# Optimization experiments

Hardware: AMD Instinct MI355X
Metric: run time of the kernel (lower is better)

Reference implementation:

```python
import jax, jax.numpy as jnp
import numpy as np

EPS = 1e-12

def _l2norm(x):
    # F.normalize(p=2, dim=-1) semantics: x / max(||x||, eps)
    n = jnp.sqrt(jnp.sum(x * x, axis=-1, keepdims=True))
    return x / jnp.maximum(n, EPS)

def _split_heads(x, h):
    b, l, d = x.shape
    return x.reshape(b, l, h, d // h).transpose(0, 2, 1, 3)  # (B,H,L,dh)

def _join_heads(x):
    b, h, l, dh = x.shape
    return x.transpose(0, 2, 1, 3).reshape(b, l, h * dh)

def setup_inputs() -> dict:
    key = jax.random.key(0)
    B, L, D = 4, 4096, 1024
    ks = jax.random.split(key, 12)
    s = 1.0 / np.sqrt(D)
    inp = {
        "queries": jax.random.normal(ks[0], (B, L, D), jnp.float32),
        "values": jax.random.normal(ks[1], (B, L, D), jnp.float32),
        "keys": jax.random.normal(ks[2], (B, L, D), jnp.float32),
        "key_attention_mask": jnp.ones((B, L), jnp.float32),
        "Wq": jax.random.uniform(ks[3], (D, D), jnp.float32, -s, s),
        "bq": jax.random.uniform(ks[4], (D,), jnp.float32, -s, s),
        "Wk": jax.random.uniform(ks[5], (D, D), jnp.float32, -s, s),
        "bk": jax.random.uniform(ks[6], (D,), jnp.float32, -s, s),
        "Wv": jax.random.uniform(ks[7], (D, D), jnp.float32, -s, s),
        "bv": jax.random.uniform(ks[8], (D,), jnp.float32, -s, s),
        "Wo": jax.random.uniform(ks[9], (D, D), jnp.float32, -s, s),
        "bo": jax.random.uniform(ks[10], (D,), jnp.float32, -s, s),
    }
    return inp

def reference(queries, values, keys, key_attention_mask, Wq, bq, Wk, bk, Wv, bv, Wo, bo):
    nhead = 16
    L2 = keys.shape[1]
    qp = jnp.einsum('bld,ed->ble', queries, Wq) + bq
    kp = jnp.einsum('bld,ed->ble', keys, Wk) + bk
    vp = jnp.einsum('bld,ed->ble', values, Wv) + bv
    Q = _split_heads(qp, nhead)   # (B,H,L1,dh)
    K = _split_heads(kp, nhead)   # (B,H,L2,dh)
    V = _split_heads(vp, nhead)   # (B,H,L2,dh)
    V_minus = jnp.minimum(V, 0.0)
    V_plus = jnp.maximum(V, 0.0)
    Q = jax.nn.sigmoid(Q)
    scaled_K = jax.nn.sigmoid(K) / L2
    # AmplitudeEmbedding: L2-normalize feature maps along feature dim
    Q = _l2norm(Q)
    scaled_K = _l2norm(scaled_K)
    kv_plus = jnp.einsum('bhld,bhlc,bl->bhdc', scaled_K, V_plus, key_attention_mask)
    heads_plus = _l2norm(jnp.einsum('bhld,bhdc->bhlc', Q, kv_plus))
    kv_minus = jnp.einsum('bhld,bhlc,bl->bhdc', scaled_K, V_minus, key_attention_mask)
    heads_minus = _l2norm(jnp.einsum('bhld,bhdc->bhlc', Q, kv_minus))
    out = _join_heads(heads_plus + heads_minus)  # (B,L1,D)
    return jnp.einsum('blc,dc->bld', out, Wo) + bo
```

## Files before the change

### kernel.cpp

```cpp
#include <hip/hip_runtime.h>
#include <stdint.h>

#define B_  4
#define L_  4096
#define D_  1024
#define H_  16
#define DH  64
#define M_  (B_*L_)

typedef _Float16 f16;
typedef __attribute__((ext_vector_type(8))) _Float16 f16x8;
typedef __attribute__((ext_vector_type(4))) _Float16 f16x4;
typedef __attribute__((ext_vector_type(4))) float    f32x4;

__device__ __forceinline__ void cp16(const void* g, void* l) {
  __builtin_amdgcn_global_load_lds(
      (const __attribute__((address_space(1))) void*)g,
      (__attribute__((address_space(3))) void*)l,
      16, 0, 0);
}

#define MFMA(a,b,c) __builtin_amdgcn_mfma_f32_16x16x32_f16(a,b,c,0,0,0)

#define PH_IN do { __builtin_amdgcn_s_barrier(); \
  asm volatile("s_waitcnt lgkmcnt(0)" ::: "memory"); \
  __builtin_amdgcn_sched_barrier(0); \
  __builtin_amdgcn_s_setprio(1); } while (0)
#define PH_OUT do { __builtin_amdgcn_s_setprio(0); \
  __builtin_amdgcn_sched_barrier(0); \
  asm volatile("" ::: "memory"); \
  __builtin_amdgcn_s_barrier(); } while (0)
#define PH_OUT_VM(nimm) do { __builtin_amdgcn_s_setprio(0); \
  __builtin_amdgcn_sched_barrier(0); \
  asm volatile("s_waitcnt vmcnt(" #nimm ")" ::: "memory"); \
  __builtin_amdgcn_s_barrier(); } while (0)

__global__ __launch_bounds__(256) void k_cvt_f16(const float* __restrict__ x,
                                                 f16* __restrict__ y, int n8) {
  int i = blockIdx.x * 256 + threadIdx.x;
  if (i >= n8) return;
  const float4* xv = (const float4*)x;
  float4 a = xv[2*i], b = xv[2*i+1];
  f16x8 o;
  o[0]=(f16)a.x; o[1]=(f16)a.y; o[2]=(f16)a.z; o[3]=(f16)a.w;
  o[4]=(f16)b.x; o[5]=(f16)b.y; o[6]=(f16)b.z; o[7]=(f16)b.w;
  ((f16x8*)y)[i] = o;
}

__global__ __launch_bounds__(256) void k_split_w(const float* __restrict__ x,
                                                 f16* __restrict__ cat, int n4) {
  int i = blockIdx.x * 256 + threadIdx.x;
  if (i >= n4) return;
  float4 a = ((const float4*)x)[i];
  int n  = i >> 8;
  int k4 = i & 255;
  f16 h0=(f16)a.x, h1=(f16)a.y, h2=(f16)a.z, h3=(f16)a.w;
  f16x4 hv = {h0, h1, h2, h3};
  f16x4 lv = {(f16)(a.x-(float)h0), (f16)(a.y-(float)h1),
              (f16)(a.z-(float)h2), (f16)(a.w-(float)h3)};
  size_t rh = (size_t)((n >> 4) * 32 + (n & 15));
  ((f16x4*)cat)[rh * 256 + k4]        = hv;
  ((f16x4*)cat)[(rh + 16) * 256 + k4] = lv;
}

__global__ __launch_bounds__(512, 2) void k_gemm8(
    const f16* __restrict__ A, const f16* __restrict__ Bw,
    const float* __restrict__ bias, const float* __restrict__ mask,
    float* __restrict__ Cf, f16* __restrict__ Ch, int mode,
    int M, int N, int K) {
  __shared__ __align__(16) char sA[65536];
  __shared__ __align__(16) char sB[65536];
  const int t = threadIdx.x;
  const int nbn = N >> 8;
  int bid = blockIdx.x;
  {
    int cpx = (int)gridDim.x >> 3;
    bid = (bid & 7) * cpx + (bid >> 3);
  }
  const int bm = (bid / nbn) << 8;
  const int bn = (bid % nbn) << 8;
  const int lane = t & 63, wave = t >> 6;
  const int wm = wave >> 2;
  const int wn = wave & 3;
  const int fm = lane & 15, fkb = lane >> 4;

  auto SA_ = [&](int T, int buf, int half) {
#pragma unroll
    for (int q = 0; q < 2; ++q) {
      int li = (q << 9) + t;
      int row = li >> 3, cb = li & 7;
      const f16* g = A + (size_t)(bm + (half << 7) + row) * K
                       + (T << 6) + ((cb ^ (row & 7)) << 3);
      cp16(g, sA + buf * 32768 + half * 16384 + li * 16);
    }
  };
  auto SB_ = [&](int T, int buf, int half) {
#pragma unroll
    for (int q = 0; q < 2; ++q) {
      int li = (q << 9) + t;
      int row = li >> 3, cb = li & 7;
      const f16* g = Bw + (size_t)(bn + (half << 7) + row) * K
                        + (T << 6) + ((cb ^ (row & 7)) << 3);
      cp16(g, sB + buf * 32768 + half * 16384 + li * 16);
    }
  };
  auto LDA = [&](int buf, int i, int ks) -> f16x8 {
    int row = (i << 4) + fm;
    int blk = ((ks << 2) + fkb) ^ (row & 7);
    return *(const f16x8*)(sA + buf * 32768 + (wm << 14) + (row << 7) + (blk << 4));
  };
  auto LDB = [&](int buf, int j, int ks) -> f16x8 {
    int row = ((wn & 1) << 6) + (j << 4) + fm;
    int blk = ((ks << 2) + fkb) ^ (row & 7);
    return *(const f16x8*)(sB + buf * 32768 + ((wn >> 1) << 14) + (row << 7) + (blk << 4));
  };

  f32x4 acc[8][4] = {};

  SA_(0, 0, 0); SA_(0, 0, 1);
  SB_(0, 0, 0); SB_(0, 0, 1);
  SB_(1, 1, 0); SB_(1, 1, 1);
  asm volatile("s_waitcnt vmcnt(4)" ::: "memory");
  __builtin_amdgcn_s_barrier();

  const int NI = K >> 7;
  for (int it = 0; it < NI; ++it) {
    const bool nl = (it != NI - 1);
    const int t2 = 2 * it + 2, t3 = 2 * it + 3;
    f16x8 aL[4][2], aH[4][2], bA[2][2], bB[2][2];

#pragma unroll
    for (int i = 0; i < 4; ++i) { aL[i][0] = LDA(0,i,0); aL[i][1] = LDA(0,i,1); }
#pragma unroll
    for (int j = 0; j < 2; ++j) { bA[j][0] = LDB(0,j,0); bA[j][1] = LDB(0,j,1); }
    SA_(2*it+1, 1, 0);
    PH_IN;
#pragma unroll
    for (int i = 0; i < 4; ++i)
#pragma unroll
      for (int j = 0; j < 2; ++j) {
        acc[i][j] = MFMA(aL[i][0], bA[j][0], acc[i][j]);
        acc[i][j] = MFMA(aL[i][1], bA[j][1], acc[i][j]);
      }
    PH_OUT;
#pragma unroll
    for (int j = 0; j < 2; ++j) { bB[j][0] = LDB(0,j+2,0); bB[j][1] = LDB(0,j+2,1); }
    SA_(2*it+1, 1, 1);
    PH_IN;
#pragma unroll
    for (int i = 0; i < 4; ++i)
#pragma unroll
      for (int j = 0; j < 2; ++j) {
        acc[i][j+2] = MFMA(aL[i][0], bB[j][0], acc[i][j+2]);
        acc[i][j+2] = MFMA(aL[i][1], bB[j][1], acc[i][j+2]);
      }
    PH_OUT;
#pragma unroll
    for (int i = 0; i < 4; ++i) { aH[i][0] = LDA(0,i+4,0); aH[i][1] = LDA(0,i+4,1); }
    if (nl) SB_(t2, 0, 0);
    PH_IN;
#pragma unroll
    for (int i = 0; i < 4; ++i)
#pragma unroll
      for (int j = 0; j < 2; ++j) {
        acc[i+4][j] = MFMA(aH[i][0], bA[j][0], acc[i+4][j]);
        acc[i+4][j] = MFMA(aH[i][1], bA[j][1], acc[i+4][j]);
      }
    PH_OUT;
    if (nl) SB_(t2, 0, 1);
    PH_IN;
#pragma unroll
    for (int i = 0; i < 4; ++i)
#pragma unroll
      for (int j = 0; j < 2; ++j) {
        acc[i+4][j+2] = MFMA(aH[i][0], bB[j][0], acc[i+4][j+2]);
        acc[i+4][j+2] = MFMA(aH[i][1], bB[j][1], acc[i+4][j+2]);
      }
    if (nl) PH_OUT_VM(4); else PH_OUT_VM(0);
#pragma unroll
    for (int i = 0; i < 4; ++i) { aL[i][0] = LDA(1,i,0); aL[i][1] = LDA(1,i,1); }
#pragma unroll
    for (int j = 0; j < 2; ++j) { bA[j][0] = LDB(1,j,0); bA[j][1] = LDB(1,j,1); }
    if (nl) SA_(t2, 0, 0);
    PH_IN;
#pragma unroll
    for (int i = 0; i < 4; ++i)
#pragma unroll
      for (int j = 0; j < 2; ++j) {
        acc[i][j] = MFMA(aL[i][0], bA[j][0], acc[i][j]);
        acc[i][j] = MFMA(aL[i][1], bA[j][1], acc[i][j]);
      }
    PH_OUT;
#pragma unroll
    for (int j = 0; j < 2; ++j) { bB[j][0] = LDB(1,j+2,0); bB[j][1] = LDB(1,j+2,1); }
    if (nl) SA_(t2, 0, 1);
    PH_IN;
#pragma unroll
    for (int i = 0; i < 4; ++i)
#pragma unroll
      for (int j = 0; j < 2; ++j) {
        acc[i][j+2] = MFMA(aL[i][0], bB[j][0], acc[i][j+2]);
        acc[i][j+2] = MFMA(aL[i][1], bB[j][1], acc[i][j+2]);
      }
    PH_OUT;
#pragma unroll
    for (int i = 0; i < 4; ++i) { aH[i][0] = LDA(1,i+4,0); aH[i][1] = LDA(1,i+4,1); }
    if (nl) SB_(t3, 1, 0);
    PH_IN;
#pragma unroll
    for (int i = 0; i < 4; ++i)
#pragma unroll
      for (int j = 0; j < 2; ++j) {
        acc[i+4][j] = MFMA(aH[i][0], bA[j][0], acc[i+4][j]);
        acc[i+4][j] = MFMA(aH[i][1], bA[j][1], acc[i+4][j]);
      }
    PH_OUT;
    if (nl) SB_(t3, 1, 1);
    PH_IN;
#pragma unroll
    for (int i = 0; i < 4; ++i)
#pragma unroll
      for (int j = 0; j < 2; ++j) {
        acc[i+4][j+2] = MFMA(aH[i][0], bB[j][0], acc[i+4][j+2]);
        acc[i+4][j+2] = MFMA(aH[i][1], bB[j][1], acc[i+4][j+2]);
      }
    PH_OUT_VM(4);
  }

  const int cr = (lane >> 4) << 2, ccol = lane & 15;
  const int rowbase = bm + wm * 128;
  if (mode == 1) {
    const int No = N;
    float bvj[4];
#pragma unroll
    for (int j = 0; j < 4; ++j) bvj[j] = bias[bn + wn*64 + j*16 + ccol];
#pragma unroll
    for (int i = 0; i < 8; ++i)
#pragma unroll
      for (int r = 0; r < 4; ++r) {
        int gm = rowbase + i*16 + cr + r;
        float s[4], ss = 0.f;
#pragma unroll
        for (int j = 0; j < 4; ++j) {
          float v = acc[i][j][r] + bvj[j];
          s[j] = 1.0f / (1.0f + __expf(-v));
          ss += s[j] * s[j];
        }
        ss += __shfl_xor(ss, 1, 64);
        ss += __shfl_xor(ss, 2, 64);
        ss += __shfl_xor(ss, 4, 64);
        ss += __shfl_xor(ss, 8, 64);
        float sc = 1.0f / fmaxf(sqrtf(ss), 1e-12f);
        if (mask) sc *= mask[gm];
#pragma unroll
        for (int j = 0; j < 4; ++j)
          Ch[(size_t)gm * No + bn + wn*64 + j*16 + ccol] = (f16)(s[j] * sc);
      }
  } else {
    const int No = N >> 1;
#pragma unroll
    for (int j2 = 0; j2 < 2; ++j2) {
      int colp = bn + wn*64 + (2*j2)*16;
      int oc = ((colp >> 5) << 4) + ccol;
      float bv = bias[oc];
#pragma unroll
      for (int i = 0; i < 8; ++i)
#pragma unroll
        for (int r = 0; r < 4; ++r) {
          int gm = rowbase + i*16 + cr + r;
          float v = acc[i][2*j2][r] + acc[i][2*j2+1][r] + bv;
          if (mode == 2) Ch[(size_t)gm * No + oc] = (f16)v;
          else           Cf[(size_t)gm * No + oc] = v;
        }
    }
  }
}

#define SKT 72
__global__ __launch_bounds__(256) void k_kv_mfma(const f16* __restrict__ Kh,
                                                 const f16* __restrict__ Vh,
                                                 float* __restrict__ part) {
  __shared__ __align__(16) f16 sKt[64 * SKT];
  __shared__ __align__(16) f16 sVt[128 * SKT];
  int head = blockIdx.x >> 3, chunk = blockIdx.x & 7;
  int b = head >> 4, h = head & 15;
  int t = threadIdx.x, lane = t & 63, wave = t >> 6;
  int lp = t & 31, g8 = (t >> 5) << 3;
  size_t rowbase = (size_t)b * L_ + (size_t)chunk * 512;
  const f16* Kb = Kh + rowbase * D_ + h * DH;
  const f16* Vb = Vh + rowbase * D_ + h * DH;

  const int fm = lane & 15, fk = (lane >> 4) << 3;
  const int wm2 = (wave & 1) * 2;
  const int wn4 = (wave >> 1) * 4;
  f32x4 acc[2][4] = {};

  for (int l0 = 0; l0 < 512; l0 += 64) {
    __syncthreads();
    {
      const f16* r0 = Kb + (size_t)(l0 + 2*lp) * D_ + g8;
      f16x8 a0 = *(const f16x8*)r0;
      f16x8 a1 = *(const f16x8*)(r0 + D_);
#pragma unroll
      for (int j = 0; j < 8; ++j) {
        union { f16 h2[2]; uint32_t u; } pk;
        pk.h2[0] = a0[j]; pk.h2[1] = a1[j];
        *(uint32_t*)&sKt[(g8 + j) * SKT + 2*lp] = pk.u;
      }
      const f16* v0p = Vb + (size_t)(l0 + 2*lp) * D_ + g8;
      f16x8 b0 = *(const f16x8*)v0p;
      f16x8 b1 = *(const f16x8*)(v0p + D_);
#pragma unroll
      for (int j = 0; j < 8; ++j) {
        float x0 = (float)b0[j], x1 = (float)b1[j];
        union { f16 h2[2]; uint32_t u; } pp, pm;
        pp.h2[0] = (f16)fmaxf(x0, 0.f); pp.h2[1] = (f16)fmaxf(x1, 0.f);
        pm.h2[0] = (f16)fminf(x0, 0.f); pm.h2[1] = (f16)fminf(x1, 0.f);
        *(uint32_t*)&sVt[(g8 + j) * SKT + 2*lp]        = pp.u;
        *(uint32_t*)&sVt[(64 + g8 + j) * SKT + 2*lp]   = pm.u;
      }
    }
    __syncthreads();
#pragma unroll
    for (int ks = 0; ks < 2; ++ks) {
      f16x8 af[2], bf[4];
#pragma unroll
      for (int i = 0; i < 2; ++i)
        af[i] = *(const f16x8*)&sKt[((wm2+i)*16 + fm) * SKT + ks*32 + fk];
#pragma unroll
      for (int j = 0; j < 4; ++j)
        bf[j] = *(const f16x8*)&sVt[((wn4+j)*16 + fm) * SKT + ks*32 + fk];
#pragma unroll
      for (int i = 0; i < 2; ++i)
#pragma unroll
        for (int j = 0; j < 4; ++j)
          acc[i][j] = MFMA(af[i], bf[j], acc[i][j]);
    }
  }
  const int cr = (lane >> 4) << 2, ccol = lane & 15;
  float* pb = part + (size_t)(head * 8 + chunk) * 8192;
#pragma unroll
  for (int i = 0; i < 2; ++i)
#pragma unroll
    for (int j = 0; j < 4; ++j) {
      int d = (wm2 + i) * 16 + cr;
      int c2 = (wn4 + j) * 16 + ccol;
#pragma unroll
      for (int r = 0; r < 4; ++r)
        pb[(d + r) * 128 + c2] = acc[i][j][r];
    }
}

__global__ __launch_bounds__(256) void k_kv_reduce(const float* __restrict__ part,
                                                   float* __restrict__ kv) {
  int i = blockIdx.x * 256 + threadIdx.x;
  int head = i >> 13, dc = i & 8191;
  float s = 0.f;
#pragma unroll
  for (int c = 0; c < 8; ++c) s += part[(size_t)(head * 8 + c) * 8192 + dc];
  kv[i] = s;
}

__global__ __launch_bounds__(256) void k_kv_cvt(const float* __restrict__ kvb,
                                                f16* __restrict__ kvh) {
  int head = blockIdx.x, t = threadIdx.x;
  int c = t >> 1, half = t & 1;
  const float* src = kvb + (size_t)head * 8192 + half * 32 * 128 + c;
  f16* dst = kvh + (size_t)head * 8192 + c * 64 + half * 32;
  f16 buf[32];
#pragma unroll
  for (int kk = 0; kk < 32; ++kk) buf[kk] = (f16)src[kk * 128];
#pragma unroll
  for (int q = 0; q < 4; ++q) ((f16x8*)dst)[q] = *(const f16x8*)&buf[q * 8];
}

#define SH 72
__global__ __launch_bounds__(256) void k_heads_mfma(const f16* __restrict__ Qh,
                                                    const f16* __restrict__ kvh,
                                                    f16* __restrict__ O) {
  __shared__ __align__(16) f16 sQ [128 * SH];
  __shared__ __align__(16) f16 sKV[128 * SH];
  int bi = blockIdx.x;
  int head = bi >> 5, mt = bi & 31;
  int b = head >> 4, h = head & 15;
  int t = threadIdx.x, lane = t & 63, wave = t >> 6;
  size_t qbase = ((size_t)(b * L_ + mt * 128)) * D_ + h * DH;
  const f16* kvp = kvh + (size_t)head * 8192;
#pragma unroll
  for (int p = 0; p < 4; ++p) {
    int c = p * 256 + t;
    int row = c >> 3, off = (c & 7) * 8;
    f16x8 q = *(const f16x8*)(Qh + qbase + (size_t)row * D_ + off);
    *(f16x8*)&sQ[row * SH + off] = q;
    f16x8 kv8 = *(const f16x8*)(kvp + row * 64 + off);
    *(f16x8*)&sKV[row * SH + off] = kv8;
  }
  __syncthreads();

  const int fm = lane & 15, fk = (lane >> 4) << 3;
  const int wm = wave * 32;
  f32x4 acc[2][8] = {};
#pragma unroll
  for (int ks = 0; ks < 2; ++ks) {
    f16x8 a0 = *(const f16x8*)&sQ[(wm + fm) * SH + ks * 32 + fk];
    f16x8 a1 = *(const f16x8*)&sQ[(wm + 16 + fm) * SH + ks * 32 + fk];
#pragma unroll
    for (int j = 0; j < 8; ++j) {
      f16x8 bj = *(const f16x8*)&sKV[(j * 16 + fm) * SH + ks * 32 + fk];
      acc[0][j] = MFMA(a0, bj, acc[0][j]);
      acc[1][j] = MFMA(a1, bj, acc[1][j]);
    }
  }
  const int cr = (lane >> 4) << 2, ccol = lane & 15;
#pragma unroll
  for (int i = 0; i < 2; ++i)
#pragma unroll
    for (int r = 0; r < 4; ++r) {
      int row = wm + i * 16 + cr + r;
      float sp = 0.f, sm = 0.f;
#pragma unroll
      for (int j = 0; j < 4; ++j) {
        sp += acc[i][j][r] * acc[i][j][r];
        sm += acc[i][j + 4][r] * acc[i][j + 4][r];
      }
      sp += __shfl_xor(sp, 1, 64); sm += __shfl_xor(sm, 1, 64);
      sp += __shfl_xor(sp, 2, 64); sm += __shfl_xor(sm, 2, 64);
      sp += __shfl_xor(sp, 4, 64); sm += __shfl_xor(sm, 4, 64);
      sp += __shfl_xor(sp, 8, 64); sm += __shfl_xor(sm, 8, 64);
      float rp = 1.0f / fmaxf(sqrtf(sp), 1e-12f);
      float rm = 1.0f / fmaxf(sqrtf(sm), 1e-12f);
#pragma unroll
      for (int j = 0; j < 4; ++j) {
        float o = acc[i][j][r] * rp + acc[i][j + 4][r] * rm;
        O[qbase + (size_t)row * D_ + j * 16 + ccol] = (f16)o;
      }
    }
}

extern "C" void kernel_launch(void* const* d_in, const int* in_sizes, int n_in,
                              void* d_out, int out_size, void* d_ws, size_t ws_size,
                              hipStream_t stream) {
  const float* queries = (const float*)d_in[0];
  const float* values  = (const float*)d_in[1];
  const float* keys    = (const float*)d_in[2];
  const float* mask    = (const float*)d_in[3];
  const float* Wq = (const float*)d_in[4];  const float* bq = (const float*)d_in[5];
  const float* Wk = (const float*)d_in[6];  const float* bk = (const float*)d_in[7];
  const float* Wv = (const float*)d_in[8];  const float* bv = (const float*)d_in[9];
  const float* Wo = (const float*)d_in[10]; const float* bo = (const float*)d_in[11];
  float* out = (float*)d_out;

  const size_t MB = 1024ull * 1024ull;
  const size_t NEED = 160 * MB;
  if (ws_size < NEED) return;

  char* ws = (char*)d_ws;
  const size_t DD = (size_t)D_ * D_;
  f16*   Wqh  = (f16*)(ws);
  f16*   Wkh  = (f16*)(ws + 2 * MB);
  f16*   Wcv  = (f16*)(ws + 4 * MB);
  f16*   Wco  = (f16*)(ws + 8 * MB);
  f16*   Ah   = (f16*)(ws + 12 * MB);
  f16*   Qh   = (f16*)(ws + 44 * MB);
  float* kvb  = (float*)(ws + 76 * MB);
  f16*   kvh  = (f16*)(ws + 78 * MB);
  float* part = (float*)(ws + 80 * MB);
  f16*   kp   = (f16*)(ws + 96 * MB);
  f16*   vp   = (f16*)(ws + 128 * MB);

  const int DD8 = (int)(DD / 8);
  const int DD4 = (int)(DD / 4);
  k_cvt_f16<<<DD8 / 256, 256, 0, stream>>>(Wq, Wqh, DD8);
  k_cvt_f16<<<DD8 / 256, 256, 0, stream>>>(Wk, Wkh, DD8);
  k_split_w<<<DD4 / 256, 256, 0, stream>>>(Wv, Wcv, DD4);
  k_split_w<<<DD4 / 256, 256, 0, stream>>>(Wo, Wco, DD4);

  const int n8 = M_ * D_ / 8;
  const int g1 = (M_ / 256) * (1024 / 256);
  const int g2 = (M_ / 256) * (2048 / 256);

  k_cvt_f16<<<n8 / 256, 256, 0, stream>>>(queries, Ah, n8);
  k_gemm8<<<g1, 512, 0, stream>>>(Ah, Wqh, bq, nullptr, nullptr, Qh, 1, M_, 1024, 1024);
  k_cvt_f16<<<n8 / 256, 256, 0, stream>>>(keys, Ah, n8);
  k_gemm8<<<g1, 512, 0, stream>>>(Ah, Wkh, bk, mask, nullptr, kp, 1, M_, 1024, 1024);
  k_cvt_f16<<<n8 / 256, 256, 0, stream>>>(values, Ah, n8);
  k_gemm8<<<g2, 512, 0, stream>>>(Ah, Wcv, bv, nullptr, nullptr, vp, 2, M_, 2048, 1024);

  k_kv_mfma<<<64 * 8, 256, 0, stream>>>(kp, vp, part);
  k_kv_reduce<<<64 * 8192 / 256, 256, 0, stream>>>(part, kvb);
  k_kv_cvt<<<64, 256, 0, stream>>>(kvb, kvh);
  k_heads_mfma<<<64 * 32, 256, 0, stream>>>(Qh, kvh, Ah);

  k_gemm8<<<g2, 512, 0, stream>>>(Ah, Wco, bo, nullptr, out, nullptr, 3, M_, 2048, 1024);
}
```

Measured before the change: 554.6 us.

## Stage GEMM epilogues through LDS, batch Q/K GEMMs, and merge small kernels

```diff
diff --git a/kernel.cpp b/kernel.cpp
--- a/kernel.cpp
+++ b/kernel.cpp
@@ -47,10 +47,23 @@
   ((f16x8*)y)[i] = o;
 }
 
-__global__ __launch_bounds__(256) void k_split_w(const float* __restrict__ x,
-                                                 f16* __restrict__ cat, int n4) {
+__global__ __launch_bounds__(256) void k_cvt2(const float* __restrict__ x0,
+                                              f16* __restrict__ y0,
+                                              const float* __restrict__ x1,
+                                              f16* __restrict__ y1, int n8each) {
   int i = blockIdx.x * 256 + threadIdx.x;
-  if (i >= n4) return;
+  const float* x = x0; f16* y = y0;
+  if (i >= n8each) { x = x1; y = y1; i -= n8each; }
+  const float4* xv = (const float4*)x;
+  float4 a = xv[2*i], b = xv[2*i+1];
+  f16x8 o;
+  o[0]=(f16)a.x; o[1]=(f16)a.y; o[2]=(f16)a.z; o[3]=(f16)a.w;
+  o[4]=(f16)b.x; o[5]=(f16)b.y; o[6]=(f16)b.z; o[7]=(f16)b.w;
+  ((f16x8*)y)[i] = o;
+}
+
+__device__ __forceinline__ void split_one(const float* __restrict__ x,
+                                          f16* __restrict__ cat, int i) {
   float4 a = ((const float4*)x)[i];
   int n  = i >> 8;
   int k4 = i & 255;
@@ -63,18 +76,35 @@
   ((f16x4*)cat)[(rh + 16) * 256 + k4] = lv;
 }
 
-__global__ __launch_bounds__(512, 2) void k_gemm8(
-    const f16* __restrict__ A, const f16* __restrict__ Bw,
-    const float* __restrict__ bias, const float* __restrict__ mask,
-    float* __restrict__ Cf, f16* __restrict__ Ch, int mode,
-    int M, int N, int K) {
-  __shared__ __align__(16) char sA[65536];
-  __shared__ __align__(16) char sB[65536];
+__global__ __launch_bounds__(256) void k_split2(const float* __restrict__ x0,
+                                                f16* __restrict__ c0,
+                                                const float* __restrict__ x1,
+                                                f16* __restrict__ c1, int n4each) {
+  int i = blockIdx.x * 256 + threadIdx.x;
+  if (i < n4each) split_one(x0, c0, i);
+  else            split_one(x1, c1, i - n4each);
+}
+
+struct GemmJob {
+  const f16* A; const f16* Bw; const float* bias; const float* mask;
+  float* Cf; f16* Ch; int mode; int N;
+};
+
+__global__ __launch_bounds__(512, 2) void k_gemm8(GemmJob j0, GemmJob j1,
+                                                  int nblk0, int M, int K) {
+  __shared__ __align__(16) char smem[137216];
+  char* sA = smem;
+  char* sB = smem + 65536;
   const int t = threadIdx.x;
+
+  int raw = (int)blockIdx.x;
+  GemmJob J; int bid, nblk;
+  if (raw < nblk0) { J = j0; bid = raw;         nblk = nblk0; }
+  else             { J = j1; bid = raw - nblk0; nblk = (int)gridDim.x - nblk0; }
+  const int N = J.N;
   const int nbn = N >> 8;
-  int bid = blockIdx.x;
   {
-    int cpx = (int)gridDim.x >> 3;
+    int cpx = nblk >> 3;
     bid = (bid & 7) * cpx + (bid >> 3);
   }
   const int bm = (bid / nbn) << 8;
@@ -84,13 +114,15 @@
   const int wn = wave & 3;
   const int fm = lane & 15, fkb = lane >> 4;
 
+  const f16* Ab = J.A;
+  const f16* Bb = J.Bw;
   auto SA_ = [&](int T, int buf, int half) {
 #pragma unroll
     for (int q = 0; q < 2; ++q) {
       int li = (q << 9) + t;
       int row = li >> 3, cb = li & 7;
-      const f16* g = A + (size_t)(bm + (half << 7) + row) * K
-                       + (T << 6) + ((cb ^ (row & 7)) << 3);
+      const f16* g = Ab + (size_t)(bm + (half << 7) + row) * K
+                        + (T << 6) + ((cb ^ (row & 7)) << 3);
       cp16(g, sA + buf * 32768 + half * 16384 + li * 16);
     }
   };
@@ -99,7 +131,7 @@
     for (int q = 0; q < 2; ++q) {
       int li = (q << 9) + t;
       int row = li >> 3, cb = li & 7;
-      const f16* g = Bw + (size_t)(bn + (half << 7) + row) * K
+      const f16* g = Bb + (size_t)(bn + (half << 7) + row) * K
                         + (T << 6) + ((cb ^ (row & 7)) << 3);
       cp16(g, sB + buf * 32768 + half * 16384 + li * 16);
     }
@@ -229,49 +261,75 @@
 
   const int cr = (lane >> 4) << 2, ccol = lane & 15;
   const int rowbase = bm + wm * 128;
-  if (mode == 1) {
-    const int No = N;
+  float* sOut = (float*)smem;
+  if (J.mode == 1) {
     float bvj[4];
 #pragma unroll
-    for (int j = 0; j < 4; ++j) bvj[j] = bias[bn + wn*64 + j*16 + ccol];
-#pragma unroll
-    for (int i = 0; i < 8; ++i)
-#pragma unroll
-      for (int r = 0; r < 4; ++r) {
-        int gm = rowbase + i*16 + cr + r;
-        float s[4], ss = 0.f;
-#pragma unroll
-        for (int j = 0; j < 4; ++j) {
-          float v = acc[i][j][r] + bvj[j];
-          s[j] = 1.0f / (1.0f + __expf(-v));
-          ss += s[j] * s[j];
+    for (int j = 0; j < 4; ++j) bvj[j] = J.bias[bn + wn*64 + j*16 + ccol];
+    for (int h = 0; h < 2; ++h) {
+      if (wm == h) {
+#pragma unroll
+        for (int i = 0; i < 8; ++i)
+#pragma unroll
+          for (int r = 0; r < 4; ++r) {
+            int rl = i*16 + cr + r;
+            int gm = rowbase + rl;
+            float s[4], ss = 0.f;
+#pragma unroll
+            for (int j = 0; j < 4; ++j) {
+              float v = acc[i][j][r] + bvj[j];
+              s[j] = 1.0f / (1.0f + __expf(-v));
+              ss += s[j] * s[j];
+            }
+            ss += __shfl_xor(ss, 1, 64);
+            ss += __shfl_xor(ss, 2, 64);
+            ss += __shfl_xor(ss, 4, 64);
+            ss += __shfl_xor(ss, 8, 64);
+            float sc = 1.0f / fmaxf(sqrtf(ss), 1e-12f);
+            if (J.mask) sc *= J.mask[gm];
+#pragma unroll
+            for (int j = 0; j < 4; ++j)
+              sOut[rl*268 + wn*64 + j*16 + ccol] = s[j] * sc;
+          }
+      }
+      __syncthreads();
+#pragma unroll
+      for (int sp = 0; sp < 16; ++sp) {
+        int rl = sp*8 + (t >> 6);
+        int c4 = (t & 63) * 4;
+        f32x4 v = *(const f32x4*)&sOut[rl*268 + c4];
+        f16x4 o = {(f16)v[0], (f16)v[1], (f16)v[2], (f16)v[3]};
+        *(f16x4*)&J.Ch[(size_t)(bm + h*128 + rl) * N + bn + c4] = o;
+      }
+      __syncthreads();
+    }
+  } else {
+#pragma unroll
+    for (int j2 = 0; j2 < 2; ++j2) {
+      int ocl = wn*32 + j2*16 + ccol;
+      float bv = J.bias[(bn >> 1) + ocl];
+#pragma unroll
+      for (int i = 0; i < 8; ++i)
+#pragma unroll
+        for (int r = 0; r < 4; ++r) {
+          int rl = wm*128 + i*16 + cr + r;
+          sOut[rl*132 + ocl] = acc[i][2*j2][r] + acc[i][2*j2+1][r] + bv;
         }
-        ss += __shfl_xor(ss, 1, 64);
-        ss += __shfl_xor(ss, 2, 64);
-        ss += __shfl_xor(ss, 4, 64);
-        ss += __shfl_xor(ss, 8, 64);
-        float sc = 1.0f / fmaxf(sqrtf(ss), 1e-12f);
-        if (mask) sc *= mask[gm];
-#pragma unroll
-        for (int j = 0; j < 4; ++j)
-          Ch[(size_t)gm * No + bn + wn*64 + j*16 + ccol] = (f16)(s[j] * sc);
-      }
-  } else {
+    }
+    __syncthreads();
     const int No = N >> 1;
 #pragma unroll
-    for (int j2 = 0; j2 < 2; ++j2) {
-      int colp = bn + wn*64 + (2*j2)*16;
-      int oc = ((colp >> 5) << 4) + ccol;
-      float bv = bias[oc];
-#pragma unroll
-      for (int i = 0; i < 8; ++i)
-#pragma unroll
-        for (int r = 0; r < 4; ++r) {
-          int gm = rowbase + i*16 + cr + r;
-          float v = acc[i][2*j2][r] + acc[i][2*j2+1][r] + bv;
-          if (mode == 2) Ch[(size_t)gm * No + oc] = (f16)v;
-          else           Cf[(size_t)gm * No + oc] = v;
-        }
+    for (int sp = 0; sp < 16; ++sp) {
+      int rl = sp*16 + (t >> 5);
+      int c4 = (t & 31) * 4;
+      f32x4 v = *(const f32x4*)&sOut[rl*132 + c4];
+      size_t g = (size_t)(bm + rl) * No + (bn >> 1) + c4;
+      if (J.mode == 2) {
+        f16x4 o = {(f16)v[0], (f16)v[1], (f16)v[2], (f16)v[3]};
+        *(f16x4*)&J.Ch[g] = o;
+      } else {
+        *(f32x4*)&J.Cf[g] = v;
+      }
     }
   }
 }
@@ -351,25 +409,20 @@
     }
 }
 
-__global__ __launch_bounds__(256) void k_kv_reduce(const float* __restrict__ part,
-                                                   float* __restrict__ kv) {
-  int i = blockIdx.x * 256 + threadIdx.x;
-  int head = i >> 13, dc = i & 8191;
-  float s = 0.f;
-#pragma unroll
-  for (int c = 0; c < 8; ++c) s += part[(size_t)(head * 8 + c) * 8192 + dc];
-  kv[i] = s;
-}
-
-__global__ __launch_bounds__(256) void k_kv_cvt(const float* __restrict__ kvb,
-                                                f16* __restrict__ kvh) {
+__global__ __launch_bounds__(256) void k_kv_redcvt(const float* __restrict__ part,
+                                                   f16* __restrict__ kvh) {
   int head = blockIdx.x, t = threadIdx.x;
   int c = t >> 1, half = t & 1;
-  const float* src = kvb + (size_t)head * 8192 + half * 32 * 128 + c;
+  const float* src = part + (size_t)head * 8 * 8192 + half * 32 * 128 + c;
   f16* dst = kvh + (size_t)head * 8192 + c * 64 + half * 32;
   f16 buf[32];
 #pragma unroll
-  for (int kk = 0; kk < 32; ++kk) buf[kk] = (f16)src[kk * 128];
+  for (int kk = 0; kk < 32; ++kk) {
+    float s = 0.f;
+#pragma unroll
+    for (int ch = 0; ch < 8; ++ch) s += src[(size_t)ch * 8192 + kk * 128];
+    buf[kk] = (f16)s;
+  }
 #pragma unroll
   for (int q = 0; q < 4; ++q) ((f16x8*)dst)[q] = *(const f16x8*)&buf[q * 8];
 }
@@ -378,8 +431,9 @@
 __global__ __launch_bounds__(256) void k_heads_mfma(const f16* __restrict__ Qh,
                                                     const f16* __restrict__ kvh,
                                                     f16* __restrict__ O) {
-  __shared__ __align__(16) f16 sQ [128 * SH];
-  __shared__ __align__(16) f16 sKV[128 * SH];
+  __shared__ __align__(16) char hsmem[2 * 128 * SH * 2];
+  f16* sQ  = (f16*)hsmem;
+  f16* sKV = (f16*)(hsmem + 128 * SH * 2);
   int bi = blockIdx.x;
   int head = bi >> 5, mt = bi & 31;
   int b = head >> 4, h = head & 15;
@@ -411,6 +465,8 @@
       acc[1][j] = MFMA(a1, bj, acc[1][j]);
     }
   }
+  __syncthreads();
+  float* sOf = (float*)hsmem;
   const int cr = (lane >> 4) << 2, ccol = lane & 15;
 #pragma unroll
   for (int i = 0; i < 2; ++i)
@@ -430,11 +486,18 @@
       float rp = 1.0f / fmaxf(sqrtf(sp), 1e-12f);
       float rm = 1.0f / fmaxf(sqrtf(sm), 1e-12f);
 #pragma unroll
-      for (int j = 0; j < 4; ++j) {
-        float o = acc[i][j][r] * rp + acc[i][j + 4][r] * rm;
-        O[qbase + (size_t)row * D_ + j * 16 + ccol] = (f16)o;
-      }
-    }
+      for (int j = 0; j < 4; ++j)
+        sOf[row * 68 + j * 16 + ccol] = acc[i][j][r] * rp + acc[i][j + 4][r] * rm;
+    }
+  __syncthreads();
+#pragma unroll
+  for (int sp = 0; sp < 8; ++sp) {
+    int rl = sp * 16 + (t >> 4);
+    int c4 = (t & 15) * 4;
+    f32x4 v = *(const f32x4*)&sOf[rl * 68 + c4];
+    f16x4 o = {(f16)v[0], (f16)v[1], (f16)v[2], (f16)v[3]};
+    *(f16x4*)&O[qbase + (size_t)rl * D_ + c4] = o;
+  }
 }
 
 extern "C" void kernel_launch(void* const* d_in, const int* in_sizes, int n_in,
@@ -462,7 +525,6 @@
   f16*   Wco  = (f16*)(ws + 8 * MB);
   f16*   Ah   = (f16*)(ws + 12 * MB);
   f16*   Qh   = (f16*)(ws + 44 * MB);
-  float* kvb  = (float*)(ws + 76 * MB);
   f16*   kvh  = (f16*)(ws + 78 * MB);
   float* part = (float*)(ws + 80 * MB);
   f16*   kp   = (f16*)(ws + 96 * MB);
@@ -470,26 +532,34 @@
 
   const int DD8 = (int)(DD / 8);
   const int DD4 = (int)(DD / 4);
-  k_cvt_f16<<<DD8 / 256, 256, 0, stream>>>(Wq, Wqh, DD8);
-  k_cvt_f16<<<DD8 / 256, 256, 0, stream>>>(Wk, Wkh, DD8);
-  k_split_w<<<DD4 / 256, 256, 0, stream>>>(Wv, Wcv, DD4);
-  k_split_w<<<DD4 / 256, 256, 0, stream>>>(Wo, Wco, DD4);
-
-  const int n8 = M_ * D_ / 8;
-  const int g1 = (M_ / 256) * (1024 / 256);
-  const int g2 = (M_ / 256) * (2048 / 256);
-
-  k_cvt_f16<<<n8 / 256, 256, 0, stream>>>(queries, Ah, n8);
-  k_gemm8<<<g1, 512, 0, stream>>>(Ah, Wqh, bq, nullptr, nullptr, Qh, 1, M_, 1024, 1024);
-  k_cvt_f16<<<n8 / 256, 256, 0, stream>>>(keys, Ah, n8);
-  k_gemm8<<<g1, 512, 0, stream>>>(Ah, Wkh, bk, mask, nullptr, kp, 1, M_, 1024, 1024);
-  k_cvt_f16<<<n8 / 256, 256, 0, stream>>>(values, Ah, n8);
-  k_gemm8<<<g2, 512, 0, stream>>>(Ah, Wcv, bv, nullptr, nullptr, vp, 2, M_, 2048, 1024);
+  const int n8  = M_ * D_ / 8;
+
+  f16* q16 = Ah;
+  f16* k16 = vp;
+  f16* v16 = Ah;
+
+  k_cvt2 <<<2 * DD8 / 256, 256, 0, stream>>>(Wq, Wqh, Wk, Wkh, DD8);
+  k_split2<<<2 * DD4 / 256, 256, 0, stream>>>(Wv, Wcv, Wo, Wco, DD4);
+
+  k_cvt2<<<2 * n8 / 256, 256, 0, stream>>>(queries, q16, keys, k16, n8);
+  {
+    GemmJob jq = { q16, Wqh, bq, nullptr, nullptr, Qh, 1, 1024 };
+    GemmJob jk = { k16, Wkh, bk, mask,    nullptr, kp, 1, 1024 };
+    k_gemm8<<<512, 512, 0, stream>>>(jq, jk, 256, M_, 1024);
+  }
+
+  k_cvt_f16<<<n8 / 256, 256, 0, stream>>>(values, v16, n8);
+  {
+    GemmJob jv = { v16, Wcv, bv, nullptr, nullptr, vp, 2, 2048 };
+    k_gemm8<<<512, 512, 0, stream>>>(jv, jv, 512, M_, 1024);
+  }
 
   k_kv_mfma<<<64 * 8, 256, 0, stream>>>(kp, vp, part);
-  k_kv_reduce<<<64 * 8192 / 256, 256, 0, stream>>>(part, kvb);
-  k_kv_cvt<<<64, 256, 0, stream>>>(kvb, kvh);
+  k_kv_redcvt<<<64, 256, 0, stream>>>(part, kvh);
   k_heads_mfma<<<64 * 32, 256, 0, stream>>>(Qh, kvh, Ah);
 
-  k_gemm8<<<g2, 512, 0, stream>>>(Ah, Wco, bo, nullptr, out, nullptr, 3, M_, 2048, 1024);
-}
+  {
+    GemmJob jo = { Ah, Wco, bo, nullptr, out, nullptr, 3, 2048 };
+    k_gemm8<<<512, 512, 0, stream>>>(jo, jo, 512, M_, 1024);
+  }
+}
```

New measurement: 504.3 us. 9.1% less time.
